# Kernel optimization log

Hardware: AMD Instinct MI355X
Metric: run time of the kernel (lower is better)

Reference implementation:

```python
import jax, jax.numpy as jnp
import numpy as np

D_MODEL = 2048
N_HEADS = 16
N_KV_HEADS = 4
D_K = D_MODEL // N_HEADS  # 128
N_REP = N_HEADS // N_KV_HEADS
WINDOW = 128  # current_window_size default
RMS_EPS = 1e-8
ROPE_BASE = 10000.0
MASK_FILL = -10000.0


def _rmsnorm(x, w):
    rms = jnp.sqrt(jnp.mean(x * x, axis=-1, keepdims=True) + RMS_EPS)
    return x / rms * w


def _rope(x, cos, sin):
    # x: [B, S, H, d_k]; cos/sin: [S, d_k//2]; pairs are interleaved (..., -1, 2)
    B, S, H, dk = x.shape
    xr = x.reshape(B, S, H, dk // 2, 2)
    x1, x2 = xr[..., 0], xr[..., 1]
    c = cos[None, :, None, :]
    s = sin[None, :, None, :]
    o1 = x1 * c - x2 * s
    o2 = x1 * s + x2 * c
    return jnp.stack([o1, o2], axis=-1).reshape(B, S, H, dk)


def setup_inputs() -> dict:
    key = jax.random.key(0)
    ks = jax.random.split(key, 10)
    B, S = 2, 2048
    std = 1.0 / np.sqrt(D_MODEL)
    inp = {
        "x": jax.random.normal(ks[0], (B, S, D_MODEL), dtype=jnp.float32),
        "Wq": jax.random.normal(ks[1], (D_MODEL, D_MODEL), dtype=jnp.float32) * std,
        "bq": jnp.zeros((D_MODEL,), dtype=jnp.float32),
        "Wk": jax.random.normal(ks[2], (N_KV_HEADS * D_K, D_MODEL), dtype=jnp.float32) * std,
        "bk": jnp.zeros((N_KV_HEADS * D_K,), dtype=jnp.float32),
        "Wv": jax.random.normal(ks[3], (N_KV_HEADS * D_K, D_MODEL), dtype=jnp.float32) * std,
        "bv": jnp.zeros((N_KV_HEADS * D_K,), dtype=jnp.float32),
        "Wo": jax.random.normal(ks[4], (D_MODEL, D_MODEL), dtype=jnp.float32) * std,
        "bo": jnp.zeros((D_MODEL,), dtype=jnp.float32),
        "qn_w": jnp.ones((D_K,), dtype=jnp.float32),
        "kn_w": jnp.ones((D_K,), dtype=jnp.float32),
        "scale": jnp.asarray(1.0 / np.sqrt(D_K), dtype=jnp.float32),
    }
    return inp


def reference(x, Wq, bq, Wk, bk, Wv, bv, Wo, bo, qn_w, kn_w, scale):
    B, S, D = x.shape
    # projections
    q = (x @ Wq.T + bq).reshape(B, S, N_HEADS, D_K)
    k = (x @ Wk.T + bk).reshape(B, S, N_KV_HEADS, D_K)
    v = (x @ Wv.T + bv).reshape(B, S, N_KV_HEADS, D_K)
    # per-head RMSNorm
    q = _rmsnorm(q, qn_w)
    k = _rmsnorm(k, kn_w)
    # RoPE
    inv_freq = 1.0 / (ROPE_BASE ** (jnp.arange(0, D_K, 2, dtype=jnp.float32) / D_K))
    t = jnp.arange(S, dtype=jnp.float32)
    freqs = t[:, None] * inv_freq[None, :]  # [S, D_K//2]
    cos, sin = jnp.cos(freqs), jnp.sin(freqs)
    q = _rope(q, cos, sin)
    k = _rope(k, cos, sin)
    # [B, H, S, d_k]
    q = q.transpose(0, 2, 1, 3)
    k = k.transpose(0, 2, 1, 3)
    v = v.transpose(0, 2, 1, 3)
    # GQA repeat (repeat_interleave on head dim)
    k = jnp.repeat(k, N_REP, axis=1)
    v = jnp.repeat(v, N_REP, axis=1)
    # dense sliding-window path (window < seq_len)
    scores = jnp.einsum("bhqd,bhkd->bhqk", q, k) * scale
    idx = jnp.arange(S)
    causal = idx[:, None] < idx[None, :]  # triu diag=1
    local = jnp.abs(idx[:, None] - idx[None, :]) > (WINDOW // 2)
    mask = causal | local
    scores = jnp.where(mask[None, None, :, :], MASK_FILL, scores)
    attn = jax.nn.softmax(scores, axis=-1)
    out = jnp.einsum("bhqk,bhkd->bhqd", attn, v)
    out = out.transpose(0, 2, 1, 3).reshape(B, S, D)
    return out @ Wo.T + bo
```

## Files before the change

kernel.cpp:

```cpp
#include <hip/hip_runtime.h>

#define BATCH 2
#define SEQ 2048
#define DMODEL 2048
#define NHEADS 16
#define NKV 4
#define DK 128
#define WINH 64
#define NQKV 3072

typedef unsigned short ushort_t;
typedef __attribute__((ext_vector_type(8))) __bf16 bf16x8;
typedef __attribute__((ext_vector_type(4))) float f32x4;

__device__ __forceinline__ float b2f(ushort_t u) {
    union { unsigned int i; float f; } v; v.i = ((unsigned int)u) << 16; return v.f;
}
__device__ __forceinline__ ushort_t f2b(float f) {
    union { float f; unsigned int i; } v; v.f = f;
    unsigned int r = v.i + 0x7FFFu + ((v.i >> 16) & 1u);
    return (ushort_t)(r >> 16);
}

__device__ __forceinline__ void gload_lds16(const ushort_t* g, ushort_t* l) {
    __builtin_amdgcn_global_load_lds(
        (__attribute__((address_space(1))) void*)(void*)const_cast<ushort_t*>(g),
        (__attribute__((address_space(3))) void*)l, 16, 0, 0);
}

__global__ __launch_bounds__(256) void prep(
    const float* __restrict__ x,  const float* __restrict__ Wq,
    const float* __restrict__ Wk, const float* __restrict__ Wv,
    const float* __restrict__ Wo, const float* __restrict__ bq,
    const float* __restrict__ bk, const float* __restrict__ bv,
    ushort_t* __restrict__ xb, ushort_t* __restrict__ wdst,
    float* __restrict__ bqkv, float2* __restrict__ rtab)
{
    const int blk = blockIdx.x;
    const int tid = threadIdx.x;
    if (blk < 4096) {
        int i = blk * 256 + tid;
        float4 a = *((const float4*)x + i * 2);
        float4 b = *((const float4*)x + i * 2 + 1);
        ushort_t o[8] = { f2b(a.x), f2b(a.y), f2b(a.z), f2b(a.w),
                          f2b(b.x), f2b(b.y), f2b(b.z), f2b(b.w) };
        *((uint4*)xb + i) = *(const uint4*)o;
    } else if (blk < 9216) {
        int i = (blk - 4096) * 256 + tid;
        int row = i >> 8, c8 = i & 255;
        const float* src;
        if      (row < 2048) src = Wq + (size_t)row * 2048;
        else if (row < 2560) src = Wk + (size_t)(row - 2048) * 2048;
        else if (row < 3072) src = Wv + (size_t)(row - 2560) * 2048;
        else                 src = Wo + (size_t)(row - 3072) * 2048;
        float4 a = *((const float4*)src + c8 * 2);
        float4 b = *((const float4*)src + c8 * 2 + 1);
        ushort_t o[8] = { f2b(a.x), f2b(a.y), f2b(a.z), f2b(a.w),
                          f2b(b.x), f2b(b.y), f2b(b.z), f2b(b.w) };
        *((uint4*)wdst + i) = *(const uint4*)o;
    } else if (blk < 9228) {
        int i = (blk - 9216) * 256 + tid;
        if (i < 2048) bqkv[i] = bq[i];
        else if (i < 2560) bqkv[i] = bk[i - 2048];
        else if (i < 3072) bqkv[i] = bv[i - 2560];
    } else {
        int i = (blk - 9228) * 256 + tid;
        int s = i >> 6, dd = i & 63;
        float invfreq = exp2f(-(float)(2 * dd) * (13.287712379549449f / 128.0f));
        float ang = (float)s * invfreq;
        rtab[i] = make_float2(cosf(ang), sinf(ang));
    }
}

__global__ __launch_bounds__(256) void gemm_qkv(
    const ushort_t* __restrict__ A, const ushort_t* __restrict__ W,
    const float* __restrict__ bias, ushort_t* __restrict__ C,
    int M, int N, int K)
{
    __shared__ __attribute__((aligned(16))) ushort_t sA[8192];
    __shared__ __attribute__((aligned(16))) ushort_t sB[8192];

    const int tid  = threadIdx.x;
    const int lane = tid & 63;
    const int wave = tid >> 6;
    const int nbn  = N >> 7;

    int nwg = gridDim.x;
    int bid = blockIdx.x;
    int nb  = (nwg & 7) ? bid : ((bid & 7) * (nwg >> 3) + (bid >> 3));
    const int bm = nb / nbn;
    const int bn = nb % nbn;
    const int m0 = bm << 7, n0 = bn << 7;
    const int wm = wave >> 1, wn = wave & 1;

    f32x4 acc[4][4] = {};

    const int frow = lane & 15;
    const int kg   = lane >> 4;

    const ushort_t* gA[4]; const ushort_t* gB[4];
    ushort_t* lA[4]; ushort_t* lB[4];
#pragma unroll
    for (int j = 0; j < 4; ++j) {
        int t = wave * 4 + j;
        int c = t * 64 + lane;
        int r = c >> 3, s = c & 7;
        int ksrc = s ^ (r & 7);
        gA[j] = A + (size_t)(m0 + r) * K + ksrc * 8;
        gB[j] = W + (size_t)(n0 + r) * K + ksrc * 8;
        lA[j] = sA + t * 512;
        lB[j] = sB + t * 512;
    }

    for (int k0 = 0; k0 < K; k0 += 64) {
        if (k0) __syncthreads();
#pragma unroll
        for (int j = 0; j < 4; ++j) gload_lds16(gA[j] + k0, lA[j]);
#pragma unroll
        for (int j = 0; j < 4; ++j) gload_lds16(gB[j] + k0, lB[j]);
        __syncthreads();

        bf16x8 af[4][2], bfr[4][2];
#pragma unroll
        for (int mi = 0; mi < 4; ++mi)
#pragma unroll
            for (int kk = 0; kk < 2; ++kk) {
                int r = (wm << 6) + (mi << 4) + frow;
                int sl = (kk * 4 + kg) ^ (r & 7);
                af[mi][kk] = *(const bf16x8*)(sA + (r * 8 + sl) * 8);
            }
#pragma unroll
        for (int ni = 0; ni < 4; ++ni)
#pragma unroll
            for (int kk = 0; kk < 2; ++kk) {
                int r = (wn << 6) + (ni << 4) + frow;
                int sl = (kk * 4 + kg) ^ (r & 7);
                bfr[ni][kk] = *(const bf16x8*)(sB + (r * 8 + sl) * 8);
            }
#pragma unroll
        for (int kk = 0; kk < 2; ++kk)
#pragma unroll
            for (int mi = 0; mi < 4; ++mi)
#pragma unroll
                for (int ni = 0; ni < 4; ++ni)
                    acc[mi][ni] = __builtin_amdgcn_mfma_f32_16x16x32_bf16(
                        af[mi][kk], bfr[ni][kk], acc[mi][ni], 0, 0, 0);
    }

    const int orow = (lane >> 4) << 2;
    const int ocol = lane & 15;
#pragma unroll
    for (int ni = 0; ni < 4; ++ni) {
        int col = n0 + (wn << 6) + (ni << 4) + ocol;
        float bvf = bias[col];
#pragma unroll
        for (int mi = 0; mi < 4; ++mi) {
#pragma unroll
            for (int r = 0; r < 4; ++r) {
                int row = m0 + (wm << 6) + (mi << 4) + orow + r;
                C[(size_t)row * N + col] = f2b(acc[mi][ni][r] + bvf);
            }
        }
    }
}

__global__ __launch_bounds__(512) void gemm_out_ks(
    const ushort_t* __restrict__ A, const ushort_t* __restrict__ W,
    const float* __restrict__ bias, float* __restrict__ C,
    int M, int N, int K)
{
    __shared__ __attribute__((aligned(16))) unsigned char smem[65536];
    ushort_t* sA = (ushort_t*)smem;
    ushort_t* sB = (ushort_t*)(smem + 16384);
    float*    red = (float*)smem;

    const int tid  = threadIdx.x;
    const int lane = tid & 63;
    const int wave = tid >> 6;
    const int g    = wave >> 2;
    const int q    = wave & 3;
    const int wm   = q >> 1, wn = q & 1;
    const int nbn  = N >> 7;

    int nwg = gridDim.x;
    int bid = blockIdx.x;
    int nb  = (nwg & 7) ? bid : ((bid & 7) * (nwg >> 3) + (bid >> 3));
    const int bm = nb / nbn;
    const int bn = nb % nbn;
    const int m0 = bm << 7, n0 = bn << 7;

    f32x4 acc[4][4] = {};

    const int frow = lane & 15;
    const int kg   = lane >> 4;

    const ushort_t* gA[2]; const ushort_t* gB[2];
    ushort_t* lA[2]; ushort_t* lB[2];
#pragma unroll
    for (int j = 0; j < 2; ++j) {
        int t = wave * 2 + j;
        int c = t * 64 + lane;
        int r = c >> 3, s = c & 7;
        int ksrc = s ^ (r & 7);
        gA[j] = A + (size_t)(m0 + r) * K + ksrc * 8;
        gB[j] = W + (size_t)(n0 + r) * K + ksrc * 8;
        lA[j] = sA + t * 512;
        lB[j] = sB + t * 512;
    }

    for (int k0 = 0; k0 < K; k0 += 64) {
        if (k0) __syncthreads();
#pragma unroll
        for (int j = 0; j < 2; ++j) gload_lds16(gA[j] + k0, lA[j]);
#pragma unroll
        for (int j = 0; j < 2; ++j) gload_lds16(gB[j] + k0, lB[j]);
        __syncthreads();

        bf16x8 af[4], bfr[4];
#pragma unroll
        for (int mi = 0; mi < 4; ++mi) {
            int r = (wm << 6) + (mi << 4) + frow;
            int sl = ((g << 2) + kg) ^ (r & 7);
            af[mi] = *(const bf16x8*)(sA + (r * 8 + sl) * 8);
        }
#pragma unroll
        for (int ni = 0; ni < 4; ++ni) {
            int r = (wn << 6) + (ni << 4) + frow;
            int sl = ((g << 2) + kg) ^ (r & 7);
            bfr[ni] = *(const bf16x8*)(sB + (r * 8 + sl) * 8);
        }
#pragma unroll
        for (int mi = 0; mi < 4; ++mi)
#pragma unroll
            for (int ni = 0; ni < 4; ++ni)
                acc[mi][ni] = __builtin_amdgcn_mfma_f32_16x16x32_bf16(
                    af[mi], bfr[ni], acc[mi][ni], 0, 0, 0);
    }

    __syncthreads();
    if (g == 1) {
#pragma unroll
        for (int mi = 0; mi < 4; ++mi)
#pragma unroll
            for (int ni = 0; ni < 4; ++ni)
                *(f32x4*)(red + q * 4096 + (mi * 4 + ni) * 256 + lane * 4) =
                    acc[mi][ni];
    }
    __syncthreads();

    if (g == 0) {
        const int orow = (lane >> 4) << 2;
        const int ocol = lane & 15;
#pragma unroll
        for (int ni = 0; ni < 4; ++ni) {
            int col = n0 + (wn << 6) + (ni << 4) + ocol;
            float bvf = bias[col];
#pragma unroll
            for (int mi = 0; mi < 4; ++mi) {
                f32x4 other = *(const f32x4*)(red + q * 4096 + (mi * 4 + ni) * 256 + lane * 4);
#pragma unroll
                for (int r = 0; r < 4; ++r) {
                    int row = m0 + (wm << 6) + (mi << 4) + orow + r;
                    C[(size_t)row * N + col] = acc[mi][ni][r] + other[r] + bvf;
                }
            }
        }
    }
}

__global__ __launch_bounds__(256) void attn_mfma(
    const ushort_t* __restrict__ qkv, const float* __restrict__ qn_w,
    const float* __restrict__ kn_w, const float* __restrict__ scp,
    const float2* __restrict__ rtab, ushort_t* __restrict__ ao)
{
    __shared__ __attribute__((aligned(16))) ushort_t sK[16384];
    __shared__ __attribute__((aligned(16))) ushort_t sVT[16384];

    const int tid  = threadIdx.x;
    const int lane = tid & 63;
    const int w    = tid >> 6;
    const int c    = lane & 15;
    const int g    = lane >> 4;

    const int blk = blockIdx.x;
    const int qt  = blk & 31;
    const int h   = (blk >> 5) & 15;
    const int b   = blk >> 9;
    const int kvh = h >> 2;
    const int i0  = qt << 6;
    const int jb  = i0 - 64;
    const float scale = scp[0];

    bf16x8 aq[4];
    {
        const int srow = i0 + w * 16 + c;
        const ushort_t* qp = qkv + ((size_t)(b * 2048 + srow)) * NQKV
                                 + h * 128 + g * 8;
        float xv[4][8];
        float ss = 0.f;
#pragma unroll
        for (int ks = 0; ks < 4; ++ks) {
            ushort_t raw[8];
            *(uint4*)raw = *(const uint4*)(qp + ks * 32);
#pragma unroll
            for (int j = 0; j < 8; ++j) {
                float xf = b2f(raw[j]);
                xv[ks][j] = xf;
                ss += xf * xf;
            }
        }
        ss += __shfl_xor(ss, 16, 64);
        ss += __shfl_xor(ss, 32, 64);
        float inv = rsqrtf(ss * (1.0f / 128.0f) + 1e-8f) * scale;
#pragma unroll
        for (int ks = 0; ks < 4; ++ks) {
            ushort_t outb[8];
#pragma unroll
            for (int jj = 0; jj < 4; ++jj) {
                int d = ks * 32 + g * 8 + 2 * jj;
                float2 w2 = *(const float2*)(qn_w + d);
                float x0 = xv[ks][2 * jj]     * inv * w2.x;
                float x1 = xv[ks][2 * jj + 1] * inv * w2.y;
                float2 cs = rtab[(srow << 6) + (d >> 1)];
                outb[2 * jj]     = f2b(x0 * cs.x - x1 * cs.y);
                outb[2 * jj + 1] = f2b(x0 * cs.y + x1 * cs.x);
            }
            aq[ks] = *(const bf16x8*)outb;
        }
    }

    const ushort_t* kvb = qkv + ((size_t)b * 2048) * NQKV + 2048 + kvh * 128;
#pragma unroll
    for (int it = 0; it < 8; ++it) {
        int idx = it * 256 + tid;
        int rr = idx >> 4, cc = idx & 15;
        int j = jb + rr; if (j < 0) j = 0;
        ushort_t raw[8];
        *(uint4*)raw = *(const uint4*)(kvb + (size_t)j * NQKV + cc * 8);
        float xv[8];
        float ss = 0.f;
#pragma unroll
        for (int jj = 0; jj < 8; ++jj) {
            xv[jj] = b2f(raw[jj]);
            ss += xv[jj] * xv[jj];
        }
        ss += __shfl_xor(ss, 1, 64);
        ss += __shfl_xor(ss, 2, 64);
        ss += __shfl_xor(ss, 4, 64);
        ss += __shfl_xor(ss, 8, 64);
        float inv = rsqrtf(ss * (1.0f / 128.0f) + 1e-8f);
        ushort_t outb[8];
#pragma unroll
        for (int jj = 0; jj < 4; ++jj) {
            int d = cc * 8 + 2 * jj;
            float2 w2 = *(const float2*)(kn_w + d);
            float x0 = xv[2 * jj]     * inv * w2.x;
            float x1 = xv[2 * jj + 1] * inv * w2.y;
            float2 cs = rtab[(j << 6) + (d >> 1)];
            outb[2 * jj]     = f2b(x0 * cs.x - x1 * cs.y);
            outb[2 * jj + 1] = f2b(x0 * cs.y + x1 * cs.x);
        }
        int f2v = (rr & 15) ^ ((rr >> 3) & 15);
        *(uint4*)(sK + (rr * 16 + (cc ^ f2v)) * 8) = *(const uint4*)outb;
    }
#pragma unroll
    for (int it = 0; it < 4; ++it) {
        int task = it * 256 + tid;
        int pp = task >> 4, d8 = task & 15;
        int j0 = jb + 2 * pp;     if (j0 < 0) j0 = 0;
        int j1 = jb + 2 * pp + 1; if (j1 < 0) j1 = 0;
        ushort_t e0[8]; *(uint4*)e0 = *(const uint4*)(kvb + (size_t)j0 * NQKV + 512 + d8 * 8);
        ushort_t e1[8]; *(uint4*)e1 = *(const uint4*)(kvb + (size_t)j1 * NQKV + 512 + d8 * 8);
        int cc = pp >> 2;
#pragma unroll
        for (int jj = 0; jj < 8; ++jj) {
            int rr = d8 * 8 + jj;
            int f2v = (rr & 15) ^ ((rr >> 3) & 15);
            unsigned int word = (unsigned int)e0[jj] | ((unsigned int)e1[jj] << 16);
            *(unsigned int*)(sVT + (rr * 16 + (cc ^ f2v)) * 8 + (pp & 3) * 2) = word;
        }
    }
    __syncthreads();

    f32x4 s[8] = {};
#pragma unroll
    for (int nt = 0; nt < 8; ++nt) {
        int rr = nt * 16 + c;
        int f2v = (rr & 15) ^ ((rr >> 3) & 15);
#pragma unroll
        for (int ks = 0; ks < 4; ++ks) {
            bf16x8 bk = *(const bf16x8*)(sK + (rr * 16 + ((ks * 4 + g) ^ f2v)) * 8);
            s[nt] = __builtin_amdgcn_mfma_f32_16x16x32_bf16(aq[ks], bk, s[nt], 0, 0, 0);
        }
    }

    float linv[4];
#pragma unroll
    for (int r = 0; r < 4; ++r) {
        int qb = w * 16 + g * 4 + r;
#pragma unroll
        for (int nt = 0; nt < 8; ++nt) {
            int jl = nt * 16 + c;
            bool valid = (jl >= qb) && (jl <= qb + 64) && (i0 + jl >= 64);
            s[nt][r] = valid ? s[nt][r] : -1e30f;
        }
        float m = s[0][r];
#pragma unroll
        for (int nt = 1; nt < 8; ++nt) m = fmaxf(m, s[nt][r]);
#pragma unroll
        for (int off = 1; off <= 8; off <<= 1) m = fmaxf(m, __shfl_xor(m, off, 64));
        float sum = 0.f;
#pragma unroll
        for (int nt = 0; nt < 8; ++nt) {
            float e = __expf(s[nt][r] - m);
            s[nt][r] = e;
            sum += e;
        }
#pragma unroll
        for (int off = 1; off <= 8; off <<= 1) sum += __shfl_xor(sum, off, 64);
        linv[r] = 1.0f / sum;
    }

    __syncthreads();
    float* Pw = (float*)sK + w * 2048;
#pragma unroll
    for (int nt = 0; nt < 8; ++nt) {
#pragma unroll
        for (int r = 0; r < 4; ++r) {
            int q = g * 4 + r;
            int chunk = nt * 4 + (c >> 2);
            Pw[q * 128 + ((chunk ^ (q & 7)) * 4) + (c & 3)] = s[nt][r];
        }
    }

    f32x4 o[8] = {};
#pragma unroll
    for (int kt = 0; kt < 4; ++kt) {
        float pf[8];
#pragma unroll
        for (int e = 0; e < 2; ++e) {
            int chunk = kt * 8 + g * 2 + e;
            f32x4 v4 = *(const f32x4*)(Pw + c * 128 + ((chunk ^ (c & 7)) * 4));
            pf[e * 4 + 0] = v4[0]; pf[e * 4 + 1] = v4[1];
            pf[e * 4 + 2] = v4[2]; pf[e * 4 + 3] = v4[3];
        }
        ushort_t pb[8];
#pragma unroll
        for (int j = 0; j < 8; ++j) pb[j] = f2b(pf[j]);
        bf16x8 pa = *(const bf16x8*)pb;
#pragma unroll
        for (int dt = 0; dt < 8; ++dt) {
            int rr = dt * 16 + c;
            int f2v = (rr & 15) ^ ((rr >> 3) & 15);
            bf16x8 bv = *(const bf16x8*)(sVT + (rr * 16 + ((kt * 4 + g) ^ f2v)) * 8);
            o[dt] = __builtin_amdgcn_mfma_f32_16x16x32_bf16(pa, bv, o[dt], 0, 0, 0);
        }
    }

    const size_t orow0 = (size_t)(b * 2048 + i0 + w * 16);
#pragma unroll
    for (int dt = 0; dt < 8; ++dt) {
#pragma unroll
        for (int r = 0; r < 4; ++r) {
            int q = g * 4 + r;
            ao[(orow0 + q) * 2048 + h * 128 + dt * 16 + c] = f2b(o[dt][r] * linv[r]);
        }
    }
}

extern "C" void kernel_launch(void* const* d_in, const int* in_sizes, int n_in,
                              void* d_out, int out_size, void* d_ws, size_t ws_size,
                              hipStream_t stream)
{
    const float* x   = (const float*)d_in[0];
    const float* Wq  = (const float*)d_in[1];
    const float* bq  = (const float*)d_in[2];
    const float* Wk  = (const float*)d_in[3];
    const float* bk  = (const float*)d_in[4];
    const float* Wv  = (const float*)d_in[5];
    const float* bv  = (const float*)d_in[6];
    const float* Wo  = (const float*)d_in[7];
    const float* bo  = (const float*)d_in[8];
    const float* qnw = (const float*)d_in[9];
    const float* knw = (const float*)d_in[10];
    const float* scp = (const float*)d_in[11];
    float* out = (float*)d_out;

    const int M = BATCH * SEQ;
    ushort_t* xb    = (ushort_t*)d_ws;
    ushort_t* qkv0  = xb   + (size_t)M * DMODEL;
    ushort_t* Wqkvb = qkv0 + (size_t)M * NQKV;
    ushort_t* Wob   = Wqkvb + (size_t)NQKV * DMODEL;
    float*    bqkv  = (float*)(Wob + (size_t)DMODEL * DMODEL);
    float2*   rtab  = (float2*)(bqkv + 3072);
    ushort_t* ao    = xb;
    (void)ws_size; (void)in_sizes; (void)n_in; (void)out_size;

    prep<<<dim3(9740), 256, 0, stream>>>(x, Wq, Wk, Wv, Wo, bq, bk, bv,
                                         xb, Wqkvb, bqkv, rtab);
    gemm_qkv<<<dim3((M / 128) * (NQKV / 128)), 256, 0, stream>>>(
        xb, Wqkvb, bqkv, qkv0, M, NQKV, DMODEL);
    attn_mfma<<<dim3(BATCH * NHEADS * (SEQ / 64)), 256, 0, stream>>>(
        qkv0, qnw, knw, scp, rtab, ao);
    gemm_out_ks<<<dim3((M / 128) * (DMODEL / 128)), 512, 0, stream>>>(
        ao, Wob, bo, out, M, DMODEL, DMODEL);
}
```

Before: 139.7 us.

## Use 256x256 double-buffered tiles with 512 threads for QKV GEMM

Replaces the 128x128 QKV projection GEMM with a 256x256 output tile computed by 8 waves. K-tiles are double-buffered in 128KB of dynamic LDS so the next tile's global-to-LDS loads overlap the current tile's MFMAs, and only one barrier is used per iteration. The larger tile raises operand reuse per LDS load. The trade-off is that the grid shrinks to 192 workgroups, fewer than the CU count, and the large LDS footprint limits each CU to one workgroup.

```diff
diff --git a/kernel.cpp b/kernel.cpp
--- a/kernel.cpp
+++ b/kernel.cpp
@@ -72,93 +72,103 @@
     }
 }
 
-__global__ __launch_bounds__(256) void gemm_qkv(
+__global__ __launch_bounds__(512) void gemm_qkv_256(
     const ushort_t* __restrict__ A, const ushort_t* __restrict__ W,
     const float* __restrict__ bias, ushort_t* __restrict__ C,
     int M, int N, int K)
 {
-    __shared__ __attribute__((aligned(16))) ushort_t sA[8192];
-    __shared__ __attribute__((aligned(16))) ushort_t sB[8192];
+    extern __shared__ __attribute__((aligned(16))) ushort_t smem[];
 
     const int tid  = threadIdx.x;
     const int lane = tid & 63;
     const int wave = tid >> 6;
-    const int nbn  = N >> 7;
+    const int wm   = wave >> 2;
+    const int wn   = wave & 3;
+    const int nbn  = N >> 8;
 
     int nwg = gridDim.x;
     int bid = blockIdx.x;
     int nb  = (nwg & 7) ? bid : ((bid & 7) * (nwg >> 3) + (bid >> 3));
     const int bm = nb / nbn;
     const int bn = nb % nbn;
-    const int m0 = bm << 7, n0 = bn << 7;
-    const int wm = wave >> 1, wn = wave & 1;
-
-    f32x4 acc[4][4] = {};
+    const int m0 = bm << 8, n0 = bn << 8;
+
+    f32x4 acc[8][4] = {};
 
     const int frow = lane & 15;
     const int kg   = lane >> 4;
 
     const ushort_t* gA[4]; const ushort_t* gB[4];
-    ushort_t* lA[4]; ushort_t* lB[4];
+    int lofs[4];
 #pragma unroll
     for (int j = 0; j < 4; ++j) {
-        int t = wave * 4 + j;
-        int c = t * 64 + lane;
+        int c = j * 512 + wave * 64 + lane;
         int r = c >> 3, s = c & 7;
         int ksrc = s ^ (r & 7);
         gA[j] = A + (size_t)(m0 + r) * K + ksrc * 8;
         gB[j] = W + (size_t)(n0 + r) * K + ksrc * 8;
-        lA[j] = sA + t * 512;
-        lB[j] = sB + t * 512;
-    }
-
-    for (int k0 = 0; k0 < K; k0 += 64) {
-        if (k0) __syncthreads();
-#pragma unroll
-        for (int j = 0; j < 4; ++j) gload_lds16(gA[j] + k0, lA[j]);
-#pragma unroll
-        for (int j = 0; j < 4; ++j) gload_lds16(gB[j] + k0, lB[j]);
+        lofs[j] = (j * 512 + wave * 64) * 8;
+    }
+
+    const int nt = K >> 6;
+#pragma unroll
+    for (int j = 0; j < 4; ++j) gload_lds16(gA[j], smem + lofs[j]);
+#pragma unroll
+    for (int j = 0; j < 4; ++j) gload_lds16(gB[j], smem + 32768 + lofs[j]);
+    __syncthreads();
+
+    for (int t = 0; t < nt; ++t) {
+        const int cur = t & 1;
+        if (t + 1 < nt) {
+            const int nxt = cur ^ 1;
+            const int ko = (t + 1) << 6;
+#pragma unroll
+            for (int j = 0; j < 4; ++j)
+                gload_lds16(gA[j] + ko, smem + nxt * 16384 + lofs[j]);
+#pragma unroll
+            for (int j = 0; j < 4; ++j)
+                gload_lds16(gB[j] + ko, smem + 32768 + nxt * 16384 + lofs[j]);
+        }
+
+        const ushort_t* bufA = smem + cur * 16384;
+        const ushort_t* bufB = smem + 32768 + cur * 16384;
+#pragma unroll
+        for (int kk = 0; kk < 2; ++kk) {
+            bf16x8 af[8], bf[4];
+#pragma unroll
+            for (int mf = 0; mf < 8; ++mf) {
+                int r = wm * 128 + mf * 16 + frow;
+                int pos = r * 8 + ((kk * 4 + kg) ^ (r & 7));
+                af[mf] = *(const bf16x8*)(bufA + pos * 8);
+            }
+#pragma unroll
+            for (int nf = 0; nf < 4; ++nf) {
+                int r = wn * 64 + nf * 16 + frow;
+                int pos = r * 8 + ((kk * 4 + kg) ^ (r & 7));
+                bf[nf] = *(const bf16x8*)(bufB + pos * 8);
+            }
+#pragma unroll
+            for (int mf = 0; mf < 8; ++mf)
+#pragma unroll
+                for (int nf = 0; nf < 4; ++nf)
+                    acc[mf][nf] = __builtin_amdgcn_mfma_f32_16x16x32_bf16(
+                        af[mf], bf[nf], acc[mf][nf], 0, 0, 0);
+        }
         __syncthreads();
-
-        bf16x8 af[4][2], bfr[4][2];
-#pragma unroll
-        for (int mi = 0; mi < 4; ++mi)
-#pragma unroll
-            for (int kk = 0; kk < 2; ++kk) {
-                int r = (wm << 6) + (mi << 4) + frow;
-                int sl = (kk * 4 + kg) ^ (r & 7);
-                af[mi][kk] = *(const bf16x8*)(sA + (r * 8 + sl) * 8);
-            }
-#pragma unroll
-        for (int ni = 0; ni < 4; ++ni)
-#pragma unroll
-            for (int kk = 0; kk < 2; ++kk) {
-                int r = (wn << 6) + (ni << 4) + frow;
-                int sl = (kk * 4 + kg) ^ (r & 7);
-                bfr[ni][kk] = *(const bf16x8*)(sB + (r * 8 + sl) * 8);
-            }
-#pragma unroll
-        for (int kk = 0; kk < 2; ++kk)
-#pragma unroll
-            for (int mi = 0; mi < 4; ++mi)
-#pragma unroll
-                for (int ni = 0; ni < 4; ++ni)
-                    acc[mi][ni] = __builtin_amdgcn_mfma_f32_16x16x32_bf16(
-                        af[mi][kk], bfr[ni][kk], acc[mi][ni], 0, 0, 0);
     }
 
     const int orow = (lane >> 4) << 2;
     const int ocol = lane & 15;
 #pragma unroll
-    for (int ni = 0; ni < 4; ++ni) {
-        int col = n0 + (wn << 6) + (ni << 4) + ocol;
+    for (int nf = 0; nf < 4; ++nf) {
+        int col = n0 + wn * 64 + nf * 16 + ocol;
         float bvf = bias[col];
 #pragma unroll
-        for (int mi = 0; mi < 4; ++mi) {
+        for (int mf = 0; mf < 8; ++mf) {
 #pragma unroll
             for (int r = 0; r < 4; ++r) {
-                int row = m0 + (wm << 6) + (mi << 4) + orow + r;
-                C[(size_t)row * N + col] = f2b(acc[mi][ni][r] + bvf);
+                int row = m0 + wm * 128 + mf * 16 + orow + r;
+                C[(size_t)row * N + col] = f2b(acc[mf][nf][r] + bvf);
             }
         }
     }
@@ -496,9 +506,12 @@
     ushort_t* ao    = xb;
     (void)ws_size; (void)in_sizes; (void)n_in; (void)out_size;
 
+    hipFuncSetAttribute((const void*)gemm_qkv_256,
+                        hipFuncAttributeMaxDynamicSharedMemorySize, 131072);
+
     prep<<<dim3(9740), 256, 0, stream>>>(x, Wq, Wk, Wv, Wo, bq, bk, bv,
                                          xb, Wqkvb, bqkv, rtab);
-    gemm_qkv<<<dim3((M / 128) * (NQKV / 128)), 256, 0, stream>>>(
+    gemm_qkv_256<<<dim3((M / 256) * (NQKV / 256)), 512, 131072, stream>>>(
         xb, Wqkvb, bqkv, qkv0, M, NQKV, DMODEL);
     attn_mfma<<<dim3(BATCH * NHEADS * (SEQ / 64)), 256, 0, stream>>>(
         qkv0, qnw, knw, scp, rtab, ao);
```

Result: no change. 139.6 us (-0.0%).
